# Kernel optimization log

Hardware: AMD Instinct MI355X
Metric: run time of the kernel (lower is better)

The kernel has to match this reference:

```python
import jax, jax.numpy as jnp
import numpy as np

B, C, H, W = 4, 256, 128, 128
WS = 16                      # window_size
DA = 64                      # dim_attn = dim // head_dim_reduce_ratio
MID = 1024                   # mid_dim = dim * ratio
SCALE = DA ** -0.5           # num_heads=1 -> dim_head = DA


def setup_inputs() -> dict:
    key = jax.random.key(0)
    ks = jax.random.split(key, 14)
    def w(k, shape, std=0.02):
        return jax.random.normal(k, shape, dtype=jnp.float32) * std
    return {
        "x": jax.random.normal(ks[0], (B, C, H, W), dtype=jnp.float32),
        "q_w": w(ks[1], (DA, C)),
        "q_s": jax.random.uniform(ks[2], (DA,), minval=0.5, maxval=1.5),
        "q_b": w(ks[3], (DA,), 0.1),
        "k_w": w(ks[4], (DA, C)),
        "k_s": jax.random.uniform(ks[5], (DA,), minval=0.5, maxval=1.5),
        "k_b": w(ks[6], (DA,), 0.1),
        "vg_w": w(ks[7], (2 * MID, C)),
        "vg_s": jax.random.uniform(ks[8], (2 * MID,), minval=0.5, maxval=1.5),
        "vg_b": w(ks[9], (2 * MID,), 0.1),
        "p_w": w(ks[10], (C, MID)),
        "p_s": jax.random.uniform(ks[11], (C,), minval=0.5, maxval=1.5),
        "p_b": w(ks[12], (C,), 0.1),
    }


def _conv1x1_bn(xf, w, s, b):
    # xf: [Bw, Cin, N]; 1x1 conv + folded BatchNorm (per-channel affine)
    return jnp.einsum("oc,bcn->bon", w, xf) * s[:, None] + b[:, None]


def reference(x, q_w, q_s, q_b, k_w, k_s, k_b, vg_w, vg_s, vg_b, p_w, p_s, p_b):
    nH, nW = H // WS, W // WS
    # window_partition: [B,C,H,W] -> [B*nH*nW, C, WS, WS]
    xw = x.reshape(B, C, nH, WS, nW, WS).transpose(0, 2, 4, 1, 3, 5)
    xf = xw.reshape(B * nH * nW, C, WS * WS)  # [Bw, C, N]

    # v_gate conv -> sigmoid applied to BOTH halves (matches source)
    vg = jax.nn.sigmoid(_conv1x1_bn(xf, vg_w, vg_s, vg_b))   # [Bw, 2*MID, N]
    v, gate = jnp.split(vg, 2, axis=1)                        # [Bw, MID, N] each

    q = _conv1x1_bn(xf, q_w, q_s, q_b) * SCALE                # [Bw, DA, N]
    k = _conv1x1_bn(xf, k_w, k_s, k_b)                        # [Bw, DA, N]

    attn = jax.nn.softmax(jnp.einsum("bcn,bcm->bnm", q, k), axis=-1)  # [Bw, N, N]
    out = jnp.einsum("bcm,bnm->bcn", v, attn)                 # v @ attn^T -> [Bw, MID, N]
    out = out * gate
    out = _conv1x1_bn(out, p_w, p_s, p_b)                     # [Bw, C, N]

    # window_reverse: [B*nH*nW, C, WS, WS] -> [B, C, H, W]
    out = out.reshape(B, nH, nW, C, WS, WS).transpose(0, 3, 1, 4, 2, 5)
    return out.reshape(B, C, H, W)
```

## Files before the change

kernel.cpp:

```cpp
#include <hip/hip_runtime.h>
#include <hip/hip_bf16.h>

#define B_    4
#define C_    256
#define H_    128
#define W_    128
#define NW_   256
#define N_    256
#define DA_   64
#define MID_  1024
#define SCALE_ 0.125f

typedef __attribute__((ext_vector_type(8))) __bf16 frag8;
typedef __attribute__((ext_vector_type(4))) float  f32x4;
typedef __attribute__((ext_vector_type(4))) unsigned int u32x4;

#define MFMA(a, b, c) __builtin_amdgcn_mfma_f32_16x16x32_bf16(a, b, c, 0, 0, 0)

__device__ __forceinline__ unsigned short f2bf(float x) {
    union { float f; unsigned u; } v; v.f = x;
    unsigned r = v.u + 0x7FFFu + ((v.u >> 16) & 1u);
    return (unsigned short)(r >> 16);
}
__device__ __forceinline__ float bf2f(unsigned short h) {
    union { unsigned u; float f; } v; v.u = ((unsigned)h) << 16;
    return v.f;
}
__device__ __forceinline__ frag8 loadf8(const unsigned short* p) {
    return *reinterpret_cast<const frag8*>(p);
}

__global__ void k_wprep(const float* __restrict__ qw, const float* __restrict__ qs,
                        const float* __restrict__ kw, const float* __restrict__ ks,
                        const float* __restrict__ vgw, const float* __restrict__ vgs,
                        const float* __restrict__ pw, const float* __restrict__ ps,
                        unsigned short* __restrict__ wvg,
                        unsigned short* __restrict__ wqk,
                        unsigned short* __restrict__ wp) {
    int i = blockIdx.x * 256 + threadIdx.x;
    if (i < 2048 * 256) {
        int r = i >> 8;
        wvg[i] = f2bf(vgw[i] * vgs[r]);
        return;
    }
    int j = i - 2048 * 256;
    if (j < 128 * 256) {
        int r = j >> 8, c = j & 255;
        float v = (r < 64) ? qw[r * 256 + c] * qs[r] * SCALE_
                           : kw[(r - 64) * 256 + c] * ks[r - 64];
        wqk[j] = f2bf(v);
        return;
    }
    int m = j - 128 * 256;
    if (m < 256 * 1024) {
        int o = m >> 10;
        wp[m] = f2bf(pw[m] * ps[o]);
    }
}

__global__ void k_pack(const float* __restrict__ x, unsigned short* __restrict__ xfT) {
    __shared__ unsigned short tile[64][258];
    int wdw = blockIdx.x >> 2, cq = blockIdx.x & 3;
    int b = wdw >> 6, wh = (wdw >> 3) & 7, ww = wdw & 7;
    int tid = threadIdx.x;
    int n = tid;
    int h = wh * 16 + (n >> 4), wc = ww * 16 + (n & 15);
    const float* xb = x + ((long)(b * C_ + cq * 64)) * (H_ * W_) + h * W_ + wc;
    #pragma unroll 4
    for (int cl = 0; cl < 64; ++cl)
        tile[cl][n] = f2bf(xb[cl * H_ * W_]);
    __syncthreads();
    unsigned short* dst = xfT + (long)wdw * (N_ * C_) + cq * 64;
    int cl = tid & 63;
    #pragma unroll 4
    for (int it = 0; it < 64; ++it) {
        int nn = it * 4 + (tid >> 6);
        dst[nn * C_ + cl] = tile[cl][nn];
    }
}

__global__ __launch_bounds__(512, 4) void k_attn(const unsigned short* __restrict__ xfT,
                                                 const unsigned short* __restrict__ wqk,
                                                 const float* __restrict__ qb,
                                                 const float* __restrict__ kb,
                                                 unsigned short* __restrict__ attn) {
    __shared__ __align__(16) char smem[73728];
    unsigned short (*qT)[72] = reinterpret_cast<unsigned short(*)[72]>(smem);
    unsigned short (*kT)[72] = reinterpret_cast<unsigned short(*)[72]>(smem + 36864);
    char* wqlds = smem;
    int wdw = blockIdx.x;
    int tid = threadIdx.x, w = tid >> 6, l = tid & 63;
    int l16 = l & 15, lg = l >> 4;
    const unsigned short* xw = xfT + (long)wdw * (N_ * C_);

    {
        int srow = tid >> 2;
        int cb = (tid & 3) * 128;
        const u32x4* src = reinterpret_cast<const u32x4*>(wqk + srow * 256 + (tid & 3) * 64);
        int sw = (srow & 7) << 4;
        #pragma unroll
        for (int j = 0; j < 8; ++j)
            *reinterpret_cast<u32x4*>(wqlds + srow * 512 + ((cb + j * 16) ^ sw)) = src[j];
    }
    __syncthreads();

    f32x4 acc[8][2];
    #pragma unroll
    for (int a = 0; a < 8; ++a) {
        acc[a][0] = (f32x4){0.f, 0.f, 0.f, 0.f};
        acc[a][1] = (f32x4){0.f, 0.f, 0.f, 0.f};
    }
    for (int kk = 0; kk < 8; ++kk) {
        int c0 = kk * 32 + lg * 8;
        frag8 b0 = loadf8(xw + (32 * w + l16) * 256 + c0);
        frag8 b1 = loadf8(xw + (32 * w + 16 + l16) * 256 + c0);
        int cbyte = c0 * 2;
        #pragma unroll
        for (int rt = 0; rt < 8; ++rt) {
            int row = rt * 16 + l16;
            frag8 af = *reinterpret_cast<const frag8*>(
                wqlds + row * 512 + (cbyte ^ ((row & 7) << 4)));
            acc[rt][0] = MFMA(af, b0, acc[rt][0]);
            acc[rt][1] = MFMA(af, b1, acc[rt][1]);
        }
    }
    __syncthreads();

    #pragma unroll
    for (int rt = 0; rt < 8; ++rt) {
        int rowb = rt * 16 + lg * 4;
        bool isq = rt < 4;
        float b0 = isq ? qb[rowb + 0] * SCALE_ : kb[rowb - 64 + 0];
        float b1 = isq ? qb[rowb + 1] * SCALE_ : kb[rowb - 64 + 1];
        float b2 = isq ? qb[rowb + 2] * SCALE_ : kb[rowb - 64 + 2];
        float b3 = isq ? qb[rowb + 3] * SCALE_ : kb[rowb - 64 + 3];
        #pragma unroll
        for (int ct = 0; ct < 2; ++ct) {
            int col = 32 * w + ct * 16 + l16;
            ushort4 t;
            t.x = f2bf(acc[rt][ct][0] + b0);
            t.y = f2bf(acc[rt][ct][1] + b1);
            t.z = f2bf(acc[rt][ct][2] + b2);
            t.w = f2bf(acc[rt][ct][3] + b3);
            unsigned short* dstp = isq ? &qT[col][rowb] : &kT[col][rowb - 64];
            *reinterpret_cast<ushort4*>(dstp) = t;
        }
    }
    __syncthreads();

    #pragma unroll
    for (int pass = 0; pass < 2; ++pass) {
        int n0 = pass * 128 + w * 16;
        f32x4 a2[16];
        #pragma unroll
        for (int c = 0; c < 16; ++c) a2[c] = (f32x4){0.f, 0.f, 0.f, 0.f};
        #pragma unroll
        for (int kk = 0; kk < 2; ++kk) {
            int k0 = kk * 32 + lg * 8;
            frag8 af = loadf8(&qT[n0 + l16][k0]);
            #pragma unroll
            for (int ct = 0; ct < 16; ++ct) {
                frag8 bf = loadf8(&kT[ct * 16 + l16][k0]);
                a2[ct] = MFMA(af, bf, a2[ct]);
            }
        }
        #pragma unroll
        for (int r = 0; r < 4; ++r) {
            int n = n0 + lg * 4 + r;
            float mx = -1e30f;
            #pragma unroll
            for (int ct = 0; ct < 16; ++ct) mx = fmaxf(mx, a2[ct][r]);
            #pragma unroll
            for (int d = 1; d < 16; d <<= 1) mx = fmaxf(mx, __shfl_xor(mx, d, 64));
            float p[16], s = 0.f;
            #pragma unroll
            for (int ct = 0; ct < 16; ++ct) { p[ct] = __expf(a2[ct][r] - mx); s += p[ct]; }
            #pragma unroll
            for (int d = 1; d < 16; d <<= 1) s += __shfl_xor(s, d, 64);
            float inv = __builtin_amdgcn_rcpf(s);
            unsigned short* dst = attn + (long)wdw * (N_ * N_) + n * 256 + l16;
            #pragma unroll
            for (int ct = 0; ct < 16; ++ct) dst[ct * 16] = f2bf(p[ct] * inv);
        }
    }
}

__device__ __forceinline__ void wstage_load(u32x4 wr[4], const unsigned short* __restrict__ wvg,
                                            int mid0, int h, int tid) {
    int srow = tid >> 2;
    long grow = (srow < 64) ? (long)(mid0 + srow) : (long)(MID_ + mid0 + srow - 64);
    const u32x4* src = reinterpret_cast<const u32x4*>(wvg + grow * 256 + h * 128 + (tid & 3) * 32);
    wr[0] = src[0]; wr[1] = src[1]; wr[2] = src[2]; wr[3] = src[3];
}
__device__ __forceinline__ void wstage_write(const u32x4 wr[4], char* wlds, int tid) {
    int srow = tid >> 2;
    int cb = (tid & 3) * 64;
    int sw = (srow & 7) << 4;
    #pragma unroll
    for (int j = 0; j < 4; ++j)
        *reinterpret_cast<u32x4*>(wlds + srow * 256 + ((cb + j * 16) ^ sw)) = wr[j];
}
__device__ __forceinline__ void vg_mfma_half(const char* wlds,
                                             const unsigned short* __restrict__ xwA,
                                             const unsigned short* __restrict__ xwB,
                                             int h, int l16, int lg, f32x4 accA[8][2]) {
    #pragma unroll
    for (int kkl = 0; kkl < 4; ++kkl) {
        int c0 = h * 128 + kkl * 32 + lg * 8;
        frag8 b0 = loadf8(xwA + c0);
        frag8 b1 = loadf8(xwB + c0);
        int cbase = kkl * 64 + lg * 16;
        #pragma unroll
        for (int rt = 0; rt < 8; ++rt) {
            int row = rt * 16 + l16;
            frag8 af = *reinterpret_cast<const frag8*>(
                wlds + row * 256 + (cbase ^ ((row & 7) << 4)));
            accA[rt][0] = MFMA(af, b0, accA[rt][0]);
            accA[rt][1] = MFMA(af, b1, accA[rt][1]);
        }
    }
}

__global__ __launch_bounds__(512, 4) void k_vgpv(const unsigned short* __restrict__ xfT,
                                                 const unsigned short* __restrict__ attn,
                                                 const unsigned short* __restrict__ wvg,
                                                 const float* __restrict__ vgb,
                                                 unsigned short* __restrict__ pvg) {
    __shared__ __align__(16) unsigned short vlds[64][264];
    __shared__ __align__(16) char wlds[32768];
    __shared__ float vgb_s[256];
    int bid = blockIdx.x;
    int lane8 = bid & 7, rr = bid >> 3;
    int sub = rr & 7, winHi = rr >> 3;
    int wdw = winHi * 8 + lane8;
    int mtbase = sub * 2;

    int tid = threadIdx.x, w = tid >> 6, l = tid & 63;
    int l16 = l & 15, lg = l >> 4;
    int nb = 32 * w;
    const unsigned short* xw = xfT + (long)wdw * (N_ * C_);
    const unsigned short* xwA = xw + (nb + l16) * 256;
    const unsigned short* xwB = xw + (nb + 16 + l16) * 256;
    const unsigned short* aw = attn + (long)wdw * (N_ * N_);
    const unsigned short* awA = aw + (nb + l16) * 256;
    const unsigned short* awB = aw + (nb + 16 + l16) * 256;
    unsigned short* pw_out = pvg + (long)wdw * (N_ * MID_);

    if (tid < 256) {
        int i = tid >> 7, s = tid & 127;
        int src = (s < 64) ? ((mtbase + i) * 64 + s)
                           : (MID_ + (mtbase + i) * 64 + (s - 64));
        vgb_s[tid] = vgb[src];
    }

    int mid0_0 = mtbase * 64, mid0_1 = (mtbase + 1) * 64;
    u32x4 wr[4], wr2[4];
    wstage_load(wr, wvg, mid0_0, 0, tid);
    __syncthreads();

    #pragma unroll
    for (int i = 0; i < 2; ++i) {
        int mid0 = (i == 0) ? mid0_0 : mid0_1;

        f32x4 accA[8][2];
        #pragma unroll
        for (int a = 0; a < 8; ++a) {
            accA[a][0] = (f32x4){0.f, 0.f, 0.f, 0.f};
            accA[a][1] = (f32x4){0.f, 0.f, 0.f, 0.f};
        }

        wstage_write(wr, wlds, tid);
        wstage_load(wr2, wvg, mid0, 1, tid);
        __syncthreads();
        vg_mfma_half(wlds, xwA, xwB, 0, l16, lg, accA);
        __syncthreads();

        wstage_write(wr2, wlds, tid);
        if (i == 0) wstage_load(wr, wvg, mid0_1, 0, tid);
        __syncthreads();
        vg_mfma_half(wlds, xwA, xwB, 1, l16, lg, accA);

        unsigned gpack[4][2][2];
        #pragma unroll
        for (int rt = 0; rt < 8; ++rt) {
            #pragma unroll
            for (int ct = 0; ct < 2; ++ct) {
                int col = nb + ct * 16 + l16;
                unsigned short sgb[4];
                #pragma unroll
                for (int r = 0; r < 4; ++r) {
                    int s = rt * 16 + lg * 4 + r;
                    float bias = vgb_s[i * 128 + s];
                    float t = accA[rt][ct][r] + bias;
                    sgb[r] = f2bf(__builtin_amdgcn_rcpf(1.f + __expf(-t)));
                }
                if (rt < 4) {
                    #pragma unroll
                    for (int r = 0; r < 4; ++r)
                        vlds[rt * 16 + lg * 4 + r][col] = sgb[r];
                } else {
                    gpack[rt - 4][ct][0] = (unsigned)sgb[0] | ((unsigned)sgb[1] << 16);
                    gpack[rt - 4][ct][1] = (unsigned)sgb[2] | ((unsigned)sgb[3] << 16);
                }
            }
        }
        __syncthreads();

        f32x4 acc2[4][2];
        #pragma unroll
        for (int a = 0; a < 4; ++a) {
            acc2[a][0] = (f32x4){0.f, 0.f, 0.f, 0.f};
            acc2[a][1] = (f32x4){0.f, 0.f, 0.f, 0.f};
        }
        #pragma unroll 2
        for (int kk = 0; kk < 8; ++kk) {
            int m0 = kk * 32 + lg * 8;
            frag8 b0 = loadf8(awA + m0);
            frag8 b1 = loadf8(awB + m0);
            #pragma unroll
            for (int rt = 0; rt < 4; ++rt) {
                frag8 av = loadf8(&vlds[rt * 16 + l16][m0]);
                acc2[rt][0] = MFMA(av, b0, acc2[rt][0]);
                acc2[rt][1] = MFMA(av, b1, acc2[rt][1]);
            }
        }
        __syncthreads();

        #pragma unroll
        for (int rt = 0; rt < 4; ++rt) {
            int midb = mid0 + rt * 16 + lg * 4;
            #pragma unroll
            for (int ct = 0; ct < 2; ++ct) {
                int n = nb + ct * 16 + l16;
                unsigned g01 = gpack[rt][ct][0], g23 = gpack[rt][ct][1];
                ushort4 t;
                t.x = f2bf(acc2[rt][ct][0] * bf2f((unsigned short)(g01 & 0xffff)));
                t.y = f2bf(acc2[rt][ct][1] * bf2f((unsigned short)(g01 >> 16)));
                t.z = f2bf(acc2[rt][ct][2] * bf2f((unsigned short)(g23 & 0xffff)));
                t.w = f2bf(acc2[rt][ct][3] * bf2f((unsigned short)(g23 >> 16)));
                *reinterpret_cast<ushort4*>(pw_out + (long)n * MID_ + midb) = t;
            }
        }
    }
}

__global__ __launch_bounds__(256, 4) void k_pconv(const unsigned short* __restrict__ pvg,
                                                  const unsigned short* __restrict__ wp,
                                                  const float* __restrict__ pb,
                                                  float* __restrict__ out) {
    __shared__ __align__(16) char wplds[32768];
    __shared__ float pbs[256];
    int bid = blockIdx.x;
    int win = bid >> 2, q = bid & 3;
    int tid = threadIdx.x, w = tid >> 6, l = tid & 63;
    int l16 = l & 15, lg = l >> 4;
    int nbase = q * 64 + w * 16;
    const unsigned short* bp = pvg + ((long)win * N_ + nbase) * MID_;
    const unsigned short* wrow = wp + (long)tid * MID_;

    pbs[tid] = pb[tid];

    f32x4 acc[16];
    #pragma unroll
    for (int c = 0; c < 16; ++c) acc[c] = (f32x4){0.f, 0.f, 0.f, 0.f};

    u32x4 wr[8];
    #pragma unroll
    for (int j = 0; j < 8; ++j)
        wr[j] = *reinterpret_cast<const u32x4*>(wrow + j * 8);
    __syncthreads();

    int sw = (tid & 7) << 4;
    for (int c = 0; c < 16; ++c) {
        #pragma unroll
        for (int j = 0; j < 8; ++j)
            *reinterpret_cast<u32x4*>(wplds + tid * 128 + ((j * 16) ^ sw)) = wr[j];
        __syncthreads();
        if (c < 15) {
            #pragma unroll
            for (int j = 0; j < 8; ++j)
                wr[j] = *reinterpret_cast<const u32x4*>(wrow + (c + 1) * 64 + j * 8);
        }
        #pragma unroll
        for (int kk2 = 0; kk2 < 2; ++kk2) {
            int k0 = c * 64 + kk2 * 32 + lg * 8;
            frag8 bf = loadf8(bp + l16 * MID_ + k0);
            int slot = (kk2 * 4 + lg) * 16;
            #pragma unroll
            for (int ct = 0; ct < 16; ++ct) {
                int row = ct * 16 + l16;
                frag8 af = *reinterpret_cast<const frag8*>(
                    wplds + row * 128 + (slot ^ ((row & 7) << 4)));
                acc[ct] = MFMA(af, bf, acc[ct]);
            }
        }
        __syncthreads();
    }

    int b = win >> 6, wh = (win >> 3) & 7, ww = win & 7;
    int h = wh * 16 + q * 4 + w;
    int wc = ww * 16 + l16;
    #pragma unroll
    for (int ct = 0; ct < 16; ++ct) {
        #pragma unroll
        for (int r = 0; r < 4; ++r) {
            int cc = ct * 16 + lg * 4 + r;
            out[((long)(b * C_ + cc)) * (H_ * W_) + h * W_ + wc] = acc[ct][r] + pbs[cc];
        }
    }
}

__global__ __launch_bounds__(512, 2) void k_main(const unsigned short* __restrict__ xfT,
                                                 const unsigned short* __restrict__ attn,
                                                 const unsigned short* __restrict__ wvg,
                                                 const unsigned short* __restrict__ wp,
                                                 const float* __restrict__ vgb,
                                                 const float* __restrict__ pb,
                                                 float* __restrict__ out) {
    __shared__ __align__(16) unsigned short vlds[64][264];
    __shared__ __align__(16) unsigned short glds[64][264];
    __shared__ __align__(16) unsigned short pvgT[256][72];
    __shared__ float vgb_s[2048];
    __shared__ float pb_s[256];
    int wdw = blockIdx.x;
    int tid = threadIdx.x, w = tid >> 6, l = tid & 63;
    int l16 = l & 15, lg = l >> 4;
    int nb = 32 * w;
    const unsigned short* xw = xfT + (long)wdw * (N_ * C_);
    const unsigned short* aw = attn + (long)wdw * (N_ * N_);

    {
        float4 v = reinterpret_cast<const float4*>(vgb)[tid];
        reinterpret_cast<float4*>(vgb_s)[tid] = v;
        if (tid < 256) pb_s[tid] = pb[tid];
    }

    f32x4 acc3[16][2];
    #pragma unroll
    for (int a = 0; a < 16; ++a)
        #pragma unroll
        for (int c = 0; c < 2; ++c) acc3[a][c] = (f32x4){0.f, 0.f, 0.f, 0.f};

    __syncthreads();

    for (int mt = 0; mt < 16; ++mt) {
        int mid0 = mt * 64;
        f32x4 accA[8][2];
        #pragma unroll
        for (int a = 0; a < 8; ++a) {
            accA[a][0] = (f32x4){0.f, 0.f, 0.f, 0.f};
            accA[a][1] = (f32x4){0.f, 0.f, 0.f, 0.f};
        }
        for (int kk = 0; kk < 8; ++kk) {
            int c0 = kk * 32 + lg * 8;
            frag8 b0 = loadf8(xw + (nb + l16) * 256 + c0);
            frag8 b1 = loadf8(xw + (nb + 16 + l16) * 256 + c0);
            #pragma unroll
            for (int rt = 0; rt < 8; ++rt) {
                int s = rt * 16 + l16;
                int row = (rt < 4) ? (mid0 + s) : (MID_ + mid0 + s - 64);
                frag8 af = loadf8(wvg + row * 256 + c0);
                accA[rt][0] = MFMA(af, b0, accA[rt][0]);
                accA[rt][1] = MFMA(af, b1, accA[rt][1]);
            }
        }
        #pragma unroll
        for (int rt = 0; rt < 8; ++rt) {
            #pragma unroll
            for (int ct = 0; ct < 2; ++ct) {
                int col = nb + ct * 16 + l16;
                #pragma unroll
                for (int r = 0; r < 4; ++r) {
                    int s = rt * 16 + lg * 4 + r;
                    float bias = (rt < 4) ? vgb_s[mid0 + s] : vgb_s[MID_ + mid0 + s - 64];
                    float t = accA[rt][ct][r] + bias;
                    float sg = __builtin_amdgcn_rcpf(1.f + __expf(-t));
                    if (rt < 4) vlds[s][col] = f2bf(sg);
                    else        glds[s - 64][col] = f2bf(sg);
                }
            }
        }
        __syncthreads();

        f32x4 acc2[4][2];
        #pragma unroll
        for (int a = 0; a < 4; ++a) {
            acc2[a][0] = (f32x4){0.f, 0.f, 0.f, 0.f};
            acc2[a][1] = (f32x4){0.f, 0.f, 0.f, 0.f};
        }
        for (int kk = 0; kk < 8; ++kk) {
            int m0 = kk * 32 + lg * 8;
            frag8 b0 = loadf8(aw + (nb + l16) * 256 + m0);
            frag8 b1 = loadf8(aw + (nb + 16 + l16) * 256 + m0);
            #pragma unroll
            for (int rt = 0; rt < 4; ++rt) {
                frag8 av = loadf8(&vlds[rt * 16 + l16][m0]);
                acc2[rt][0] = MFMA(av, b0, acc2[rt][0]);
                acc2[rt][1] = MFMA(av, b1, acc2[rt][1]);
            }
        }
        {
            #pragma unroll
            for (int rt = 0; rt < 4; ++rt) {
                int midb = rt * 16 + lg * 4;
                #pragma unroll
                for (int ct = 0; ct < 2; ++ct) {
                    int n = nb + ct * 16 + l16;
                    ushort4 t;
                    t.x = f2bf(acc2[rt][ct][0] * bf2f(glds[midb + 0][n]));
                    t.y = f2bf(acc2[rt][ct][1] * bf2f(glds[midb + 1][n]));
                    t.z = f2bf(acc2[rt][ct][2] * bf2f(glds[midb + 2][n]));
                    t.w = f2bf(acc2[rt][ct][3] * bf2f(glds[midb + 3][n]));
                    *reinterpret_cast<ushort4*>(&pvgT[n][midb]) = t;
                }
            }
        }
        __syncthreads();

        #pragma unroll
        for (int kk2 = 0; kk2 < 2; ++kk2) {
            int k0 = kk2 * 32 + lg * 8;
            frag8 b0 = loadf8(&pvgT[nb + l16][k0]);
            frag8 b1 = loadf8(&pvgT[nb + 16 + l16][k0]);
            #pragma unroll
            for (int rt = 0; rt < 16; ++rt) {
                frag8 ap = loadf8(wp + (rt * 16 + l16) * 1024 + mid0 + k0);
                acc3[rt][0] = MFMA(ap, b0, acc3[rt][0]);
                acc3[rt][1] = MFMA(ap, b1, acc3[rt][1]);
            }
        }
    }

    int b = wdw >> 6, wh = (wdw >> 3) & 7, ww = wdw & 7;
    #pragma unroll
    for (int rt = 0; rt < 16; ++rt) {
        #pragma unroll
        for (int ct = 0; ct < 2; ++ct) {
            int h = wh * 16 + 2 * w + ct;
            int wc = ww * 16 + l16;
            #pragma unroll
            for (int r = 0; r < 4; ++r) {
                int c = rt * 16 + lg * 4 + r;
                out[(((long)(b * C_ + c)) * H_ + h) * W_ + wc] = acc3[rt][ct][r] + pb_s[c];
            }
        }
    }
}

extern "C" void kernel_launch(void* const* d_in, const int* in_sizes, int n_in,
                              void* d_out, int out_size, void* d_ws, size_t ws_size,
                              hipStream_t stream) {
    const float* x    = (const float*)d_in[0];
    const float* q_w  = (const float*)d_in[1];
    const float* q_s  = (const float*)d_in[2];
    const float* q_b  = (const float*)d_in[3];
    const float* k_w  = (const float*)d_in[4];
    const float* k_s  = (const float*)d_in[5];
    const float* k_b  = (const float*)d_in[6];
    const float* vg_w = (const float*)d_in[7];
    const float* vg_s = (const float*)d_in[8];
    const float* vg_b = (const float*)d_in[9];
    const float* p_w  = (const float*)d_in[10];
    const float* p_s  = (const float*)d_in[11];
    const float* p_b  = (const float*)d_in[12];

    unsigned short* xfT  = (unsigned short*)d_ws;
    unsigned short* attn = xfT + (size_t)NW_ * N_ * C_;
    unsigned short* wvg  = attn + (size_t)NW_ * N_ * N_;
    unsigned short* wqk  = wvg + 2048 * 256;
    unsigned short* wp   = wqk + 128 * 256;
    unsigned short* pvg  = wp + 256 * 1024;
    size_t base_elems = (size_t)NW_ * N_ * C_ + (size_t)NW_ * N_ * N_ +
                        2048 * 256 + 128 * 256 + 256 * 1024;
    size_t need_fused = base_elems * sizeof(unsigned short);
    size_t need_split = (base_elems + (size_t)NW_ * N_ * MID_) * sizeof(unsigned short);
    if (ws_size < need_fused) return;

    k_wprep<<<3200, 256, 0, stream>>>(q_w, q_s, k_w, k_s, vg_w, vg_s, p_w, p_s,
                                      wvg, wqk, wp);
    k_pack<<<1024, 256, 0, stream>>>(x, xfT);
    k_attn<<<NW_, 512, 0, stream>>>(xfT, wqk, q_b, k_b, attn);
    if (ws_size >= need_split) {
        k_vgpv<<<NW_ * 8, 512, 0, stream>>>(xfT, attn, wvg, vg_b, pvg);
        k_pconv<<<NW_ * 4, 256, 0, stream>>>(pvg, wp, p_b, (float*)d_out);
    } else {
        k_main<<<NW_, 512, 0, stream>>>(xfT, attn, wvg, wp, vg_b, p_b, (float*)d_out);
    }
}
```

Before: 367.6 us.

## Double k_vgpv block to 1024 threads with 16 columns per wave

Changes the v/gate plus attention-apply kernel from 8 waves that each own 32 token columns to 16 waves that each own 16 columns. The LDS weight staging loads are redistributed across the larger block, and per-wave accumulators and B-fragment loads are halved. The aim is to cut register pressure and add waves for latency hiding. In exchange, the weight fragments read from LDS are reused across fewer MFMAs per wave, so LDS read traffic per MFMA doubles, and block-wide syncs now span more waves.

```diff
diff --git a/kernel.cpp b/kernel.cpp
--- a/kernel.cpp
+++ b/kernel.cpp
@@ -185,47 +185,44 @@
     }
 }
 
-__device__ __forceinline__ void wstage_load(u32x4 wr[4], const unsigned short* __restrict__ wvg,
+__device__ __forceinline__ void wstage_load(u32x4 wr[2], const unsigned short* __restrict__ wvg,
                                             int mid0, int h, int tid) {
-    int srow = tid >> 2;
+    int srow = tid >> 3;
     long grow = (srow < 64) ? (long)(mid0 + srow) : (long)(MID_ + mid0 + srow - 64);
-    const u32x4* src = reinterpret_cast<const u32x4*>(wvg + grow * 256 + h * 128 + (tid & 3) * 32);
-    wr[0] = src[0]; wr[1] = src[1]; wr[2] = src[2]; wr[3] = src[3];
-}
-__device__ __forceinline__ void wstage_write(const u32x4 wr[4], char* wlds, int tid) {
-    int srow = tid >> 2;
-    int cb = (tid & 3) * 64;
+    const u32x4* src = reinterpret_cast<const u32x4*>(wvg + grow * 256 + h * 128 + (tid & 7) * 16);
+    wr[0] = src[0];
+    wr[1] = src[1];
+}
+__device__ __forceinline__ void wstage_write(const u32x4 wr[2], char* wlds, int tid) {
+    int srow = tid >> 3;
+    int cb = (tid & 7) * 32;
     int sw = (srow & 7) << 4;
-    #pragma unroll
-    for (int j = 0; j < 4; ++j)
-        *reinterpret_cast<u32x4*>(wlds + srow * 256 + ((cb + j * 16) ^ sw)) = wr[j];
+    *reinterpret_cast<u32x4*>(wlds + srow * 256 + (cb ^ sw)) = wr[0];
+    *reinterpret_cast<u32x4*>(wlds + srow * 256 + ((cb + 16) ^ sw)) = wr[1];
 }
 __device__ __forceinline__ void vg_mfma_half(const char* wlds,
                                              const unsigned short* __restrict__ xwA,
-                                             const unsigned short* __restrict__ xwB,
-                                             int h, int l16, int lg, f32x4 accA[8][2]) {
+                                             int h, int l16, int lg, f32x4 accA[8]) {
     #pragma unroll
     for (int kkl = 0; kkl < 4; ++kkl) {
         int c0 = h * 128 + kkl * 32 + lg * 8;
         frag8 b0 = loadf8(xwA + c0);
-        frag8 b1 = loadf8(xwB + c0);
         int cbase = kkl * 64 + lg * 16;
         #pragma unroll
         for (int rt = 0; rt < 8; ++rt) {
             int row = rt * 16 + l16;
             frag8 af = *reinterpret_cast<const frag8*>(
                 wlds + row * 256 + (cbase ^ ((row & 7) << 4)));
-            accA[rt][0] = MFMA(af, b0, accA[rt][0]);
-            accA[rt][1] = MFMA(af, b1, accA[rt][1]);
-        }
-    }
-}
-
-__global__ __launch_bounds__(512, 4) void k_vgpv(const unsigned short* __restrict__ xfT,
-                                                 const unsigned short* __restrict__ attn,
-                                                 const unsigned short* __restrict__ wvg,
-                                                 const float* __restrict__ vgb,
-                                                 unsigned short* __restrict__ pvg) {
+            accA[rt] = MFMA(af, b0, accA[rt]);
+        }
+    }
+}
+
+__global__ __launch_bounds__(1024, 4) void k_vgpv(const unsigned short* __restrict__ xfT,
+                                                  const unsigned short* __restrict__ attn,
+                                                  const unsigned short* __restrict__ wvg,
+                                                  const float* __restrict__ vgb,
+                                                  unsigned short* __restrict__ pvg) {
     __shared__ __align__(16) unsigned short vlds[64][264];
     __shared__ __align__(16) char wlds[32768];
     __shared__ float vgb_s[256];
@@ -237,13 +234,11 @@
 
     int tid = threadIdx.x, w = tid >> 6, l = tid & 63;
     int l16 = l & 15, lg = l >> 4;
-    int nb = 32 * w;
+    int nb = 16 * w;
     const unsigned short* xw = xfT + (long)wdw * (N_ * C_);
     const unsigned short* xwA = xw + (nb + l16) * 256;
-    const unsigned short* xwB = xw + (nb + 16 + l16) * 256;
     const unsigned short* aw = attn + (long)wdw * (N_ * N_);
     const unsigned short* awA = aw + (nb + l16) * 256;
-    const unsigned short* awB = aw + (nb + 16 + l16) * 256;
     unsigned short* pw_out = pvg + (long)wdw * (N_ * MID_);
 
     if (tid < 256) {
@@ -254,7 +249,7 @@
     }
 
     int mid0_0 = mtbase * 64, mid0_1 = (mtbase + 1) * 64;
-    u32x4 wr[4], wr2[4];
+    u32x4 wr[2], wr2[2];
     wstage_load(wr, wvg, mid0_0, 0, tid);
     __syncthreads();
 
@@ -262,84 +257,70 @@
     for (int i = 0; i < 2; ++i) {
         int mid0 = (i == 0) ? mid0_0 : mid0_1;
 
-        f32x4 accA[8][2];
-        #pragma unroll
-        for (int a = 0; a < 8; ++a) {
-            accA[a][0] = (f32x4){0.f, 0.f, 0.f, 0.f};
-            accA[a][1] = (f32x4){0.f, 0.f, 0.f, 0.f};
-        }
+        f32x4 accA[8];
+        #pragma unroll
+        for (int a = 0; a < 8; ++a) accA[a] = (f32x4){0.f, 0.f, 0.f, 0.f};
 
         wstage_write(wr, wlds, tid);
         wstage_load(wr2, wvg, mid0, 1, tid);
         __syncthreads();
-        vg_mfma_half(wlds, xwA, xwB, 0, l16, lg, accA);
+        vg_mfma_half(wlds, xwA, 0, l16, lg, accA);
         __syncthreads();
 
         wstage_write(wr2, wlds, tid);
         if (i == 0) wstage_load(wr, wvg, mid0_1, 0, tid);
         __syncthreads();
-        vg_mfma_half(wlds, xwA, xwB, 1, l16, lg, accA);
-
-        unsigned gpack[4][2][2];
+        vg_mfma_half(wlds, xwA, 1, l16, lg, accA);
+
+        unsigned gpack[4][2];
+        int col = nb + l16;
         #pragma unroll
         for (int rt = 0; rt < 8; ++rt) {
-            #pragma unroll
-            for (int ct = 0; ct < 2; ++ct) {
-                int col = nb + ct * 16 + l16;
-                unsigned short sgb[4];
+            unsigned short sgb[4];
+            #pragma unroll
+            for (int r = 0; r < 4; ++r) {
+                int s = rt * 16 + lg * 4 + r;
+                float bias = vgb_s[i * 128 + s];
+                float t = accA[rt][r] + bias;
+                sgb[r] = f2bf(__builtin_amdgcn_rcpf(1.f + __expf(-t)));
+            }
+            if (rt < 4) {
                 #pragma unroll
-                for (int r = 0; r < 4; ++r) {
-                    int s = rt * 16 + lg * 4 + r;
-                    float bias = vgb_s[i * 128 + s];
-                    float t = accA[rt][ct][r] + bias;
-                    sgb[r] = f2bf(__builtin_amdgcn_rcpf(1.f + __expf(-t)));
-                }
-                if (rt < 4) {
-                    #pragma unroll
-                    for (int r = 0; r < 4; ++r)
-                        vlds[rt * 16 + lg * 4 + r][col] = sgb[r];
-                } else {
-                    gpack[rt - 4][ct][0] = (unsigned)sgb[0] | ((unsigned)sgb[1] << 16);
-                    gpack[rt - 4][ct][1] = (unsigned)sgb[2] | ((unsigned)sgb[3] << 16);
-                }
-            }
-        }
-        __syncthreads();
-
-        f32x4 acc2[4][2];
-        #pragma unroll
-        for (int a = 0; a < 4; ++a) {
-            acc2[a][0] = (f32x4){0.f, 0.f, 0.f, 0.f};
-            acc2[a][1] = (f32x4){0.f, 0.f, 0.f, 0.f};
-        }
+                for (int r = 0; r < 4; ++r)
+                    vlds[rt * 16 + lg * 4 + r][col] = sgb[r];
+            } else {
+                gpack[rt - 4][0] = (unsigned)sgb[0] | ((unsigned)sgb[1] << 16);
+                gpack[rt - 4][1] = (unsigned)sgb[2] | ((unsigned)sgb[3] << 16);
+            }
+        }
+        __syncthreads();
+
+        f32x4 acc2[4];
+        #pragma unroll
+        for (int a = 0; a < 4; ++a) acc2[a] = (f32x4){0.f, 0.f, 0.f, 0.f};
         #pragma unroll 2
         for (int kk = 0; kk < 8; ++kk) {
             int m0 = kk * 32 + lg * 8;
             frag8 b0 = loadf8(awA + m0);
-            frag8 b1 = loadf8(awB + m0);
             #pragma unroll
             for (int rt = 0; rt < 4; ++rt) {
                 frag8 av = loadf8(&vlds[rt * 16 + l16][m0]);
-                acc2[rt][0] = MFMA(av, b0, acc2[rt][0]);
-                acc2[rt][1] = MFMA(av, b1, acc2[rt][1]);
-            }
-        }
-        __syncthreads();
-
+                acc2[rt] = MFMA(av, b0, acc2[rt]);
+            }
+        }
+        __syncthreads();
+
+        int n = nb + l16;
         #pragma unroll
         for (int rt = 0; rt < 4; ++rt) {
             int midb = mid0 + rt * 16 + lg * 4;
-            #pragma unroll
-            for (int ct = 0; ct < 2; ++ct) {
-                int n = nb + ct * 16 + l16;
-                unsigned g01 = gpack[rt][ct][0], g23 = gpack[rt][ct][1];
-                ushort4 t;
-                t.x = f2bf(acc2[rt][ct][0] * bf2f((unsigned short)(g01 & 0xffff)));
-                t.y = f2bf(acc2[rt][ct][1] * bf2f((unsigned short)(g01 >> 16)));
-                t.z = f2bf(acc2[rt][ct][2] * bf2f((unsigned short)(g23 & 0xffff)));
-                t.w = f2bf(acc2[rt][ct][3] * bf2f((unsigned short)(g23 >> 16)));
-                *reinterpret_cast<ushort4*>(pw_out + (long)n * MID_ + midb) = t;
-            }
+            unsigned g01 = gpack[rt][0], g23 = gpack[rt][1];
+            ushort4 t;
+            t.x = f2bf(acc2[rt][0] * bf2f((unsigned short)(g01 & 0xffff)));
+            t.y = f2bf(acc2[rt][1] * bf2f((unsigned short)(g01 >> 16)));
+            t.z = f2bf(acc2[rt][2] * bf2f((unsigned short)(g23 & 0xffff)));
+            t.w = f2bf(acc2[rt][3] * bf2f((unsigned short)(g23 >> 16)));
+            *reinterpret_cast<ushort4*>(pw_out + (long)n * MID_ + midb) = t;
         }
     }
 }
@@ -581,7 +562,7 @@
     k_pack<<<1024, 256, 0, stream>>>(x, xfT);
     k_attn<<<NW_, 512, 0, stream>>>(xfT, wqk, q_b, k_b, attn);
     if (ws_size >= need_split) {
-        k_vgpv<<<NW_ * 8, 512, 0, stream>>>(xfT, attn, wvg, vg_b, pvg);
+        k_vgpv<<<NW_ * 8, 1024, 0, stream>>>(xfT, attn, wvg, vg_b, pvg);
         k_pconv<<<NW_ * 4, 256, 0, stream>>>(pvg, wp, p_b, (float*)d_out);
     } else {
         k_main<<<NW_, 512, 0, stream>>>(xfT, attn, wvg, wp, vg_b, p_b, (float*)d_out);
```

Result: faster. 354.3 us, median of 3 (-3.6%).
